# Optimization experiments

Hardware: AMD Instinct MI355X
Metric: run time of the kernel (lower is better)

The kernel has to match this reference:

```python
import jax, jax.numpy as jnp
import numpy as np

P = 524288          # total sampled points
N_RAYS = 4096       # rays
N_FREQ = 5
N_FREQ_VIEW = 3
ACT_SHIFT = float(np.log(1.0 / (1.0 - 0.1) - 1.0))  # alpha_init = 0.1
INTERVAL = 0.5      # stepsize * voxel_size_ratio


def sin_emb(x, n_freq):
    # x: (M,3) -> (M, 3 + 6*n_freq): [x, sin(2^i x), cos(2^i x)]
    freqs = 2.0 ** jnp.arange(n_freq, dtype=x.dtype)
    parts = [x]
    for f in freqs:
        parts.append(jnp.sin(f * x))
        parts.append(jnp.cos(f * x))
    return jnp.concatenate(parts, axis=1)


def _pipeline(sampling_coor, sampling_view, raw_density, ray_id,
              wb0, bb0, wb1, bb1, wb2, bb2,
              wa0, ba0, wa1, ba1, wa2, ba2,
              w_lat, b_lat, w_view, b_view, w_c0, b_c0, w_c1, b_c1):
    relu = jax.nn.relu
    emb = sin_emb(sampling_coor, N_FREQ)                    # (P, 33)
    view_emb = sin_emb(sampling_view, N_FREQ_VIEW)[ray_id]  # (P, 21)
    # Decoder_woslot (K == 1)
    h = relu(emb @ wb0 + bb0)
    h = relu(h @ wb1 + bb1)
    h = relu(h @ wb2 + bb2)
    h = jnp.concatenate([emb, h], axis=1)                   # skip: (P, 97)
    h = relu(h @ wa0 + ba0)
    h = relu(h @ wa1 + ba1)
    h = relu(h @ wa2 + ba2)
    latent = h @ w_lat + b_lat                              # (P, 64)
    hv = relu(jnp.concatenate([latent, view_emb], axis=1) @ w_view + b_view)
    rgb_raw = relu(hv @ w_c0 + b_c0) @ w_c1 + b_c1          # (P, 3)
    rgb = (jnp.tanh(rgb_raw) + 1.0) * 0.5
    sigma = jax.nn.softplus(raw_density[0] + ACT_SHIFT)     # (P,)
    # Raw2Alpha: alpha = 1 - exp(-sigma*interval); hence log(1-alpha) = -sigma*interval
    alpha = 1.0 - jnp.exp(-sigma * INTERVAL)
    log_t = -sigma * INTERVAL
    # Alphas2Weights: per-ray exclusive cumprod of (1-alpha); ray_id is sorted
    cl = jnp.cumsum(log_t)
    excl = cl - log_t                                        # exclusive global cumsum
    base = jax.ops.segment_max(excl, ray_id, num_segments=N_RAYS)  # value at each ray start
    T = jnp.exp(excl - base[ray_id])                         # transmittance
    weights = T * alpha                                      # (P,)
    alphainv_last = jnp.exp(jax.ops.segment_sum(log_t, ray_id, num_segments=N_RAYS))
    # composite with white background
    rgb_marched = (jax.ops.segment_sum(weights[:, None] * rgb, ray_id, num_segments=N_RAYS)
                   + alphainv_last[:, None])
    return rgb_marched                                       # (N_RAYS, 3)


def setup_inputs() -> dict:
    key = jax.random.key(0)
    ks = iter(jax.random.split(key, 40))

    def w(fi, fo):
        return jax.random.normal(next(ks), (fi, fo), jnp.float32) / np.sqrt(fi).astype(np.float32)

    inp = {
        'sampling_coor': jax.random.normal(next(ks), (P, 3), jnp.float32),
        'sampling_view': jax.random.normal(next(ks), (N_RAYS, 3), jnp.float32),
        'raw_density': jax.random.normal(next(ks), (1, P), jnp.float32),
        'ray_id': jnp.sort(jax.random.randint(next(ks), (P,), 0, N_RAYS, jnp.int32)),
        'wb0': w(33, 64), 'bb0': jnp.zeros((64,), jnp.float32),
        'wb1': w(64, 64), 'bb1': jnp.zeros((64,), jnp.float32),
        'wb2': w(64, 64), 'bb2': jnp.zeros((64,), jnp.float32),
        'wa0': w(97, 64), 'ba0': jnp.zeros((64,), jnp.float32),
        'wa1': w(64, 64), 'ba1': jnp.zeros((64,), jnp.float32),
        'wa2': w(64, 64), 'ba2': jnp.zeros((64,), jnp.float32),
        'w_lat': w(64, 64), 'b_lat': jnp.zeros((64,), jnp.float32),
        'w_view': w(85, 32), 'b_view': jnp.zeros((32,), jnp.float32),
        'w_c0': w(32, 16), 'b_c0': jnp.zeros((16,), jnp.float32),
        'w_c1': w(16, 3), 'b_c1': jnp.zeros((3,), jnp.float32),
    }
    return inp


def reference(sampling_coor, sampling_view, raw_density, ray_id,
              wb0, bb0, wb1, bb1, wb2, bb2,
              wa0, ba0, wa1, ba1, wa2, ba2,
              w_lat, b_lat, w_view, b_view, w_c0, b_c0, w_c1, b_c1):
    return _pipeline(sampling_coor, sampling_view, raw_density, ray_id,
                     wb0, bb0, wb1, bb1, wb2, bb2,
                     wa0, ba0, wa1, ba1, wa2, ba2,
                     w_lat, b_lat, w_view, b_view, w_c0, b_c0, w_c1, b_c1)
```

## Files before the change

### kernel.cpp

```cpp
#include <hip/hip_runtime.h>
#include <math.h>

#define NPTS  524288
#define NRAYS 4096
#define ACT_SHIFT_F (-2.1972245773362196f)
#define INTERVAL_F  0.5f

typedef _Float16 f16x8  __attribute__((ext_vector_type(8)));
typedef __fp16   fp16x2 __attribute__((ext_vector_type(2)));
typedef float    f32x4  __attribute__((ext_vector_type(4)));
typedef float    f32x16 __attribute__((ext_vector_type(16)));
typedef int      i32x2  __attribute__((ext_vector_type(2)));
typedef unsigned u32;
typedef unsigned u32x4  __attribute__((ext_vector_type(4)));

#define MFMA32(a,b,c) __builtin_amdgcn_mfma_f32_32x32x16_f16((a),(b),(c),0,0,0)

#define FB0_H   0
#define FD1_H   3072
#define FD2_H   7168
#define FA0_H   11264
#define FD3_H   18432
#define FD4_H   22528
#define FLAT_H  26624
#define LDSW_H  30720
#define FVIEW_H 30720
#define FC0_H   33792
#define BTAB_H  34816
#define VTAB_H  35840
#define RAYTAB_H 166912

#define PREP_W    34816
#define PREP_BT   (PREP_W + 512)
#define PREP_IDS  (PREP_BT + NRAYS)
#define PREP_TOTAL (PREP_IDS + NPTS)

#define UB0  0
#define UD1  1536
#define UD2  3584
#define UA0  5632
#define UD3  9216
#define UD4  11264
#define ULAT 13312
#define LDS_U32 15360

__device__ __forceinline__ u32 pk(float a, float b) {
    fp16x2 h = __builtin_amdgcn_cvt_pkrtz(a, b);
    return __builtin_bit_cast(u32, h);
}

__device__ __forceinline__ void plswap(u32 &x, u32 &y) {
    i32x2 r = __builtin_amdgcn_permlane32_swap((int)x, (int)y, false, false);
    x = (u32)r[0]; y = (u32)r[1];
}

template<bool RELU>
__device__ __forceinline__ f16x8 reluq(f16x8 v) {
    if (RELU) {
        f16x8 z = {};
        return __builtin_elementwise_max(v, z);
    }
    return v;
}

template<bool RELU>
__device__ __forceinline__ void d2b(f32x16 a, f16x8 &blo, f16x8 &bhi) {
    u32 p0 = pk(a[0],a[1]),   p1 = pk(a[2],a[3]);
    u32 p2 = pk(a[4],a[5]),   p3 = pk(a[6],a[7]);
    plswap(p0, p2); plswap(p1, p3);
    u32x4 lo = {p0, p1, p2, p3};
    blo = reluq<RELU>(__builtin_bit_cast(f16x8, lo));
    u32 p4 = pk(a[8],a[9]),   p5 = pk(a[10],a[11]);
    u32 p6 = pk(a[12],a[13]), p7 = pk(a[14],a[15]);
    plswap(p4, p6); plswap(p5, p7);
    u32x4 hw = {p4, p5, p6, p7};
    bhi = reluq<RELU>(__builtin_bit_cast(f16x8, hw));
}

__device__ __forceinline__ f16x8 ldf(const u32* __restrict__ swl, int imm) {
    return __builtin_bit_cast(f16x8, *(const u32x4*)(swl + imm));
}

extern "C" __global__ void __launch_bounds__(256)
prep_weights(const float* __restrict__ wb0, const float* __restrict__ bb0,
             const float* __restrict__ wb1, const float* __restrict__ bb1,
             const float* __restrict__ wb2, const float* __restrict__ bb2,
             const float* __restrict__ wa0, const float* __restrict__ ba0,
             const float* __restrict__ wa1, const float* __restrict__ ba1,
             const float* __restrict__ wa2, const float* __restrict__ ba2,
             const float* __restrict__ wlat, const float* __restrict__ blat,
             const float* __restrict__ wview, const float* __restrict__ bview,
             const float* __restrict__ wc0, const float* __restrict__ bc0,
             const float* __restrict__ view, const int* __restrict__ ray_id,
             _Float16* __restrict__ pool)
{
    const int id = blockIdx.x * 256 + threadIdx.x;
    if (id >= PREP_TOTAL) return;

    if (id < PREP_W) {
        int r = id; float v = 0.f;
        if (r < 33792) {
            const float* W; int base, MT;
            if      (r < 3072)  { W = wb0;  base = 0;     MT = 2; }
            else if (r < 7168)  { W = wb1;  base = 3072;  MT = 2; }
            else if (r < 11264) { W = wb2;  base = 7168;  MT = 2; }
            else if (r < 18432) { W = wa0;  base = 11264; MT = 2; }
            else if (r < 22528) { W = wa1;  base = 18432; MT = 2; }
            else if (r < 26624) { W = wa2;  base = 22528; MT = 2; }
            else if (r < 30720) { W = wlat; base = 26624; MT = 2; }
            else                { W = wview;base = 30720; MT = 1; }
            const int e    = r - base;
            const int j    = e & 7;
            const int lane = (e >> 3) & 63;
            const int col  = lane & 31, hi = lane >> 5;
            int kc, mt;
            if (MT == 2) { kc = e >> 10; mt = (e >> 9) & 1; }
            else         { kc = e >> 9;  mt = 0; }
            const int of = mt * 32 + col;
            const int k  = kc * 16 + hi * 8 + j;
            if (W == wb0) {
                if (k < 3) v = wb0[k*64+of];
                else if (k >= 4 && k < 34) v = wb0[(k-1)*64+of];
            } else if (W == wa0) {
                if (k < 3) v = wa0[k*64+of];
                else if (k >= 4 && k < 34) v = wa0[(k-1)*64+of];
                else if (k >= 48 && k < 112) v = wa0[(k-15)*64+of];
            } else if (W == wview) {
                if (k < 64) v = wview[k*32+of];
                else { int s = k - 64;
                       if (s < 3) v = wview[(64+s)*32+of];
                       else if (s >= 4 && s < 22) v = wview[(63+s)*32+of]; }
            } else {
                if (k < 64) v = W[k*64+of];
            }
            pool[id] = (_Float16)v;
        } else {
            const int e = r - 33792;
            const int j = e & 7;
            const int lane = (e >> 3) & 63;
            const int col = lane & 31, hi = lane >> 5;
            const int kc = e >> 9;
            const int k = kc * 16 + hi * 8 + j;
            float v2 = (col < 16 && k < 32) ? wc0[k*16+col] : 0.f;
            pool[id] = (_Float16)v2;
        }
        return;
    }

    if (id < PREP_BT) {
        float* bt = (float*)(pool + BTAB_H);
        const int e = id - PREP_W; float v = 0.f;
        if (e < 448) {
            int l = e >> 6, rem = e & 63;
            int mt = rem >> 5, hi2 = (rem >> 4) & 1, q = rem & 15;
            int row = (q & 3) + 8*(q >> 2) + 4*hi2 + 32*mt;
            const float* src[7] = { bb0, bb1, bb2, ba0, ba1, ba2, blat };
            v = src[l][row];
        } else if (e < 480) {
            int t = e - 448, hi2 = t >> 4, q = t & 15;
            int row = (q & 3) + 8*(q >> 2) + 4*hi2;
            v = bview[row];
        } else if (e < 496) {
            int t = e - 480, hi2 = t >> 3, q = t & 7;
            int row = (q & 3) + 8*(q >> 2) + 4*hi2;
            v = bc0[row];
        }
        bt[e] = v;
        return;
    }

    if (id < PREP_IDS) {
        const int ray = id - PREP_BT;
        const float vx = view[3*ray+0], vy = view[3*ray+1], vz = view[3*ray+2];
        u32 w_[16];
        w_[0] = pk(vx, vy); w_[1] = pk(vz, 0.f);
#pragma unroll
        for (int f = 0; f < 3; ++f) {
            const float fac = (float)(1 << f);
            float sx = __sinf(fac*vx), cx = __cosf(fac*vx);
            float sy = __sinf(fac*vy), cy = __cosf(fac*vy);
            float sz = __sinf(fac*vz), cz = __cosf(fac*vz);
            w_[2+3*f+0] = pk(sx,sy); w_[2+3*f+1] = pk(sz,cx); w_[2+3*f+2] = pk(cy,cz);
        }
#pragma unroll
        for (int i = 11; i < 16; ++i) w_[i] = 0u;
        u32* dst = (u32*)(pool + VTAB_H) + ray * 16;
#pragma unroll
        for (int i = 0; i < 4; ++i)
            ((u32x4*)dst)[i] = (u32x4){w_[4*i], w_[4*i+1], w_[4*i+2], w_[4*i+3]};
        return;
    }

    {
        const int p = id - PREP_IDS;
        int* tab = (int*)(pool + RAYTAB_H);
        const int cur  = ray_id[p];
        const int prev = (p == 0) ? -1 : ray_id[p-1];
        for (int r = prev + 1; r <= cur; ++r) tab[r] = p;
        if (p == NPTS - 1)
            for (int r = cur + 1; r <= NRAYS; ++r) tab[r] = NPTS;
    }
}

__device__ __forceinline__ void loadBV(f32x16 (&bv)[2], const float* __restrict__ bt,
                                       int l, int hi) {
#pragma unroll
    for (int mt = 0; mt < 2; ++mt) {
        const float* p = bt + l*64 + (mt*2 + hi)*16;
#pragma unroll
        for (int i = 0; i < 4; ++i) {
            f32x4 v = *(const f32x4*)(p + 4*i);
#pragma unroll
            for (int s = 0; s < 4; ++s) bv[mt][4*i + s] = v[s];
        }
    }
}

template<bool RELU>
__device__ __forceinline__ void denseL(const u32* __restrict__ swl, int base,
                                       const f32x16 (&bv)[2], f16x8 (&b)[4][4]) {
    f16x8 W[2][4];
#pragma unroll
    for (int mt = 0; mt < 2; ++mt)
#pragma unroll
        for (int kc = 0; kc < 4; ++kc)
            W[mt][kc] = ldf(swl, base + (kc*2 + mt)*256);
#pragma unroll
    for (int t = 0; t < 4; ++t) {
        f32x16 a0 = MFMA32(W[0][0], b[t][0], bv[0]);
        f32x16 a1 = MFMA32(W[1][0], b[t][0], bv[1]);
#pragma unroll
        for (int kc = 1; kc < 4; ++kc) {
            a0 = MFMA32(W[0][kc], b[t][kc], a0);
            a1 = MFMA32(W[1][kc], b[t][kc], a1);
        }
        d2b<RELU>(a0, b[t][0], b[t][1]);
        d2b<RELU>(a1, b[t][2], b[t][3]);
    }
}

extern "C" __global__ void __launch_bounds__(512, 2)
mlp_mfma(const float* __restrict__ coor, const int* __restrict__ ray_id,
         const float* __restrict__ wc1, const float* __restrict__ bc1,
         const _Float16* __restrict__ pool, _Float16* __restrict__ rgb)
{
    __shared__ __align__(16) u32 sw[LDS_U32];
    const int tid  = threadIdx.x;
    const int lane = tid & 63;
    const int wv   = tid >> 6;
    const int col  = lane & 31;
    const int hi   = lane >> 5;
    const int wbase = blockIdx.x * 1024 + wv * 128;

    {
        const u32x4* pw = (const u32x4*)pool;
        u32x4* dw = (u32x4*)sw;
#pragma unroll
        for (int i = tid; i < LDS_U32/4; i += 512) dw[i] = pw[i];
    }

    int rid[4];
#pragma unroll
    for (int t = 0; t < 4; ++t) rid[t] = ray_id[wbase + 32*t + col];

    f16x8 E[4][3];
#pragma unroll
    for (int s = 0; s < 2; ++s) {
        const int pt = wbase + s*64 + lane;
        const float x = coor[3*pt+0], y = coor[3*pt+1], z = coor[3*pt+2];
        u32 w_[17];
        w_[0] = pk(x, y); w_[1] = pk(z, 0.f);
#pragma unroll
        for (int f = 0; f < 5; ++f) {
            const float fac = (float)(1 << f);
            float sx = __sinf(fac*x), cx = __cosf(fac*x);
            float sy = __sinf(fac*y), cy = __cosf(fac*y);
            float sz = __sinf(fac*z), cz = __cosf(fac*z);
            w_[2+3*f+0] = pk(sx,sy); w_[2+3*f+1] = pk(sz,cx); w_[2+3*f+2] = pk(cy,cz);
        }
#pragma unroll
        for (int kc = 0; kc < 2; ++kc) {
            u32 xw[4], yw[4];
#pragma unroll
            for (int i = 0; i < 4; ++i) {
                xw[i] = w_[kc*8 + i]; yw[i] = w_[kc*8 + 4 + i];
                plswap(xw[i], yw[i]);
            }
            u32x4 lo = {xw[0], xw[1], xw[2], xw[3]};
            u32x4 hw = {yw[0], yw[1], yw[2], yw[3]};
            E[2*s  ][kc] = __builtin_bit_cast(f16x8, lo);
            E[2*s+1][kc] = __builtin_bit_cast(f16x8, hw);
        }
        u32 X = w_[16], Y = 0u;
        plswap(X, Y);
        u32x4 e2a = {X, 0u, 0u, 0u}, e2b = {Y, 0u, 0u, 0u};
        E[2*s  ][2] = __builtin_bit_cast(f16x8, e2a);
        E[2*s+1][2] = __builtin_bit_cast(f16x8, e2b);
    }
    __syncthreads();

    const u32* swl = sw + lane * 4;
    const float* bt = (const float*)(pool + BTAB_H);

    f16x8 b[4][4];
    f32x16 bv[2];

    {
        f16x8 W[2][3];
#pragma unroll
        for (int mt = 0; mt < 2; ++mt)
#pragma unroll
            for (int kc = 0; kc < 3; ++kc)
                W[mt][kc] = ldf(swl, UB0 + (kc*2 + mt)*256);
        loadBV(bv, bt, 0, hi);
#pragma unroll
        for (int t = 0; t < 4; ++t) {
            f32x16 a0 = MFMA32(W[0][0], E[t][0], bv[0]);
            f32x16 a1 = MFMA32(W[1][0], E[t][0], bv[1]);
            a0 = MFMA32(W[0][1], E[t][1], a0);
            a1 = MFMA32(W[1][1], E[t][1], a1);
            a0 = MFMA32(W[0][2], E[t][2], a0);
            a1 = MFMA32(W[1][2], E[t][2], a1);
            d2b<true>(a0, b[t][0], b[t][1]);
            d2b<true>(a1, b[t][2], b[t][3]);
        }
    }

    loadBV(bv, bt, 1, hi);
    denseL<true>(swl, UD1, bv, b);
    loadBV(bv, bt, 2, hi);
    denseL<true>(swl, UD2, bv, b);

    {
        f16x8 We[2][3], Wh[2][4];
#pragma unroll
        for (int mt = 0; mt < 2; ++mt) {
#pragma unroll
            for (int kc = 0; kc < 3; ++kc)
                We[mt][kc] = ldf(swl, UA0 + (kc*2 + mt)*256);
#pragma unroll
            for (int kc = 0; kc < 4; ++kc)
                Wh[mt][kc] = ldf(swl, UA0 + ((kc+3)*2 + mt)*256);
        }
        loadBV(bv, bt, 3, hi);
#pragma unroll
        for (int t = 0; t < 4; ++t) {
            f32x16 a0 = MFMA32(We[0][0], E[t][0], bv[0]);
            f32x16 a1 = MFMA32(We[1][0], E[t][0], bv[1]);
            a0 = MFMA32(We[0][1], E[t][1], a0);
            a1 = MFMA32(We[1][1], E[t][1], a1);
            a0 = MFMA32(We[0][2], E[t][2], a0);
            a1 = MFMA32(We[1][2], E[t][2], a1);
#pragma unroll
            for (int kc = 0; kc < 4; ++kc) {
                a0 = MFMA32(Wh[0][kc], b[t][kc], a0);
                a1 = MFMA32(Wh[1][kc], b[t][kc], a1);
            }
            d2b<true>(a0, b[t][0], b[t][1]);
            d2b<true>(a1, b[t][2], b[t][3]);
        }
    }

    loadBV(bv, bt, 4, hi);
    denseL<true>(swl, UD3, bv, b);
    loadBV(bv, bt, 5, hi);
    denseL<true>(swl, UD4, bv, b);

    const _Float16* vtab = pool + VTAB_H;
    f16x8 VE[4][2];
#pragma unroll
    for (int t = 0; t < 4; ++t)
#pragma unroll
        for (int kc = 0; kc < 2; ++kc)
            VE[t][kc] = *(const f16x8*)(vtab + rid[t]*32 + kc*16 + hi*8);

    loadBV(bv, bt, 6, hi);
    denseL<false>(swl, ULAT, bv, b);

    {
        f16x8 Wv[6];
#pragma unroll
        for (int kc = 0; kc < 6; ++kc)
            Wv[kc] = *(const f16x8*)(pool + FVIEW_H + (kc*64 + lane)*8);
        f32x16 bvv;
        {
            const float* p = bt + 448 + hi*16;
#pragma unroll
            for (int i = 0; i < 4; ++i) {
                f32x4 v = *(const f32x4*)(p + 4*i);
#pragma unroll
                for (int s = 0; s < 4; ++s) bvv[4*i + s] = v[s];
            }
        }
#pragma unroll
        for (int t = 0; t < 4; ++t) {
            f32x16 a = MFMA32(Wv[0], b[t][0], bvv);
#pragma unroll
            for (int kc = 1; kc < 4; ++kc) a = MFMA32(Wv[kc], b[t][kc], a);
            a = MFMA32(Wv[4], VE[t][0], a);
            a = MFMA32(Wv[5], VE[t][1], a);
            d2b<true>(a, b[t][0], b[t][1]);
        }
    }

    {
        f16x8 Wc[2];
#pragma unroll
        for (int kc = 0; kc < 2; ++kc)
            Wc[kc] = *(const f16x8*)(pool + FC0_H + (kc*64 + lane)*8);

        f32x16 C;
        {
            f32x4 c0a = *(const f32x4*)(bt + 480 + hi*8);
            f32x4 c0b = *(const f32x4*)(bt + 480 + hi*8 + 4);
#pragma unroll
            for (int s = 0; s < 4; ++s) {
                C[s] = c0a[s]; C[4+s] = c0b[s]; C[8+s] = 0.f; C[12+s] = 0.f;
            }
        }

        float wl[24];
        {
            f32x4 w0 = *(const f32x4*)(wc1 + 12*hi);
            f32x4 w1 = *(const f32x4*)(wc1 + 12*hi + 4);
            f32x4 w2 = *(const f32x4*)(wc1 + 12*hi + 8);
            f32x4 w3 = *(const f32x4*)(wc1 + 24 + 12*hi);
            f32x4 w4 = *(const f32x4*)(wc1 + 24 + 12*hi + 4);
            f32x4 w5 = *(const f32x4*)(wc1 + 24 + 12*hi + 8);
#pragma unroll
            for (int s = 0; s < 4; ++s) {
                wl[s]    = w0[s]; wl[4+s]  = w1[s]; wl[8+s]  = w2[s];
                wl[12+s] = w3[s]; wl[16+s] = w4[s]; wl[20+s] = w5[s];
            }
        }
        const float bo0 = bc1[0], bo1 = bc1[1], bo2 = bc1[2];

#pragma unroll
        for (int t = 0; t < 4; ++t) {
            f32x16 a = MFMA32(Wc[0], b[t][0], C);
            a = MFMA32(Wc[1], b[t][1], a);
            float hc[8];
#pragma unroll
            for (int i = 0; i < 8; ++i) hc[i] = fmaxf(a[i], 0.f);

            float r0 = 0.f, r1 = 0.f, r2 = 0.f;
#pragma unroll
            for (int q = 0; q < 4; ++q) {
                r0 = fmaf(hc[q], wl[3*q+0], fmaf(hc[4+q], wl[12+3*q+0], r0));
                r1 = fmaf(hc[q], wl[3*q+1], fmaf(hc[4+q], wl[12+3*q+1], r1));
                r2 = fmaf(hc[q], wl[3*q+2], fmaf(hc[4+q], wl[12+3*q+2], r2));
            }
            r0 += __shfl_xor(r0, 32);
            r1 += __shfl_xor(r1, 32);
            r2 += __shfl_xor(r2, 32);
            if (hi == 0) {
                const float K2 = 2.8853900817779268f;
                float e0 = exp2f(K2 * (r0 + bo0));
                float e1 = exp2f(K2 * (r1 + bo1));
                float e2 = exp2f(K2 * (r2 + bo2));
                float v0 = 1.f - __builtin_amdgcn_rcpf(e0 + 1.f);
                float v1 = 1.f - __builtin_amdgcn_rcpf(e1 + 1.f);
                float v2 = 1.f - __builtin_amdgcn_rcpf(e2 + 1.f);
                const int pt = wbase + 32*t + col;
                rgb[3*pt+0] = (_Float16)v0;
                rgb[3*pt+1] = (_Float16)v1;
                rgb[3*pt+2] = (_Float16)v2;
            }
        }
    }
}

extern "C" __global__ void __launch_bounds__(256)
composite(const float* __restrict__ raw_density,
          const int*   __restrict__ rtab,
          const _Float16* __restrict__ rgb,
          float*       __restrict__ out)
{
    const int lane = threadIdx.x & 63;
    const int ray  = blockIdx.x * 4 + (threadIdx.x >> 6);

    const int start = rtab[ray];
    const int end   = rtab[ray + 1];

    float carry = 0.0f, a0 = 0.0f, a1 = 0.0f, a2 = 0.0f;

    for (int base = start; base < end; base += 64) {
        const int  idx   = base + lane;
        const bool valid = idx < end;

        float lt = 0.0f, alpha = 0.0f;
        if (valid) {
            const float xx  = raw_density[idx] + ACT_SHIFT_F;
            const float sig = fmaxf(xx, 0.0f) + log1pf(expf(-fabsf(xx)));
            lt    = -sig * INTERVAL_F;
            alpha = 1.0f - expf(lt);
        }

        float incl = lt;
#pragma unroll
        for (int d = 1; d < 64; d <<= 1) {
            const float n = __shfl_up(incl, d);
            if (lane >= d) incl += n;
        }

        const float T = expf(carry + (incl - lt));
        if (valid) {
            const float w = T * alpha;
            a0 = fmaf(w, (float)rgb[3*idx+0], a0);
            a1 = fmaf(w, (float)rgb[3*idx+1], a1);
            a2 = fmaf(w, (float)rgb[3*idx+2], a2);
        }
        carry += __shfl(incl, 63);
    }

#pragma unroll
    for (int d = 32; d > 0; d >>= 1) {
        a0 += __shfl_xor(a0, d);
        a1 += __shfl_xor(a1, d);
        a2 += __shfl_xor(a2, d);
    }

    if (lane == 0) {
        const float ainv = expf(carry);
        out[3*ray+0] = a0 + ainv;
        out[3*ray+1] = a1 + ainv;
        out[3*ray+2] = a2 + ainv;
    }
}

extern "C" void kernel_launch(void* const* d_in, const int* in_sizes, int n_in,
                              void* d_out, int out_size, void* d_ws, size_t ws_size,
                              hipStream_t stream) {
    const float* coor        = (const float*)d_in[0];
    const float* view        = (const float*)d_in[1];
    const float* raw_density = (const float*)d_in[2];
    const int*   ray_id      = (const int*)  d_in[3];
    const float* wb0  = (const float*)d_in[4];  const float* bb0  = (const float*)d_in[5];
    const float* wb1  = (const float*)d_in[6];  const float* bb1  = (const float*)d_in[7];
    const float* wb2  = (const float*)d_in[8];  const float* bb2  = (const float*)d_in[9];
    const float* wa0  = (const float*)d_in[10]; const float* ba0  = (const float*)d_in[11];
    const float* wa1  = (const float*)d_in[12]; const float* ba1  = (const float*)d_in[13];
    const float* wa2  = (const float*)d_in[14]; const float* ba2  = (const float*)d_in[15];
    const float* wlat = (const float*)d_in[16]; const float* blat = (const float*)d_in[17];
    const float* wvw  = (const float*)d_in[18]; const float* bvw  = (const float*)d_in[19];
    const float* wc0  = (const float*)d_in[20]; const float* bc0  = (const float*)d_in[21];
    const float* wc1  = (const float*)d_in[22]; const float* bc1  = (const float*)d_in[23];

    _Float16* rgb  = (_Float16*)d_ws;
    _Float16* pool = (_Float16*)((char*)d_ws + (size_t)NPTS * 3 * 2);
    const int* rtab = (const int*)(pool + RAYTAB_H);

    prep_weights<<<(PREP_TOTAL + 255) / 256, 256, 0, stream>>>(
        wb0, bb0, wb1, bb1, wb2, bb2, wa0, ba0, wa1, ba1, wa2, ba2,
        wlat, blat, wvw, bvw, wc0, bc0, view, ray_id, pool);

    mlp_mfma<<<NPTS / 1024, 512, 0, stream>>>(
        coor, ray_id, wc1, bc1, pool, rgb);

    composite<<<NRAYS / 4, 256, 0, stream>>>(raw_density, rtab, rgb, (float*)d_out);
}
```

Measured before the change: 52.01 us.

## Stage bias table in LDS, raise MFMA priority, stagger waves with sleep

The bias table is copied into shared memory next to the weights, so per-layer bias loads come from LDS instead of global memory. MFMA loops are wrapped in s_setprio(1)/s_setprio(0) so math-heavy waves get issue priority. Waves are staggered with different s_sleep delays after the barrier so their MFMA and load phases interleave. The changes add 2 KB of LDS per block and some idle time at the start of each wave.

```diff
diff --git a/kernel.cpp b/kernel.cpp
--- a/kernel.cpp
+++ b/kernel.cpp
@@ -16,14 +16,6 @@
 
 #define MFMA32(a,b,c) __builtin_amdgcn_mfma_f32_32x32x16_f16((a),(b),(c),0,0,0)
 
-#define FB0_H   0
-#define FD1_H   3072
-#define FD2_H   7168
-#define FA0_H   11264
-#define FD3_H   18432
-#define FD4_H   22528
-#define FLAT_H  26624
-#define LDSW_H  30720
 #define FVIEW_H 30720
 #define FC0_H   33792
 #define BTAB_H  34816
@@ -42,7 +34,9 @@
 #define UD3  9216
 #define UD4  11264
 #define ULAT 13312
-#define LDS_U32 15360
+#define WLDS_U32 15360
+#define BT_U32   512
+#define LDS_U32 (WLDS_U32 + BT_U32)
 
 __device__ __forceinline__ u32 pk(float a, float b) {
     fp16x2 h = __builtin_amdgcn_cvt_pkrtz(a, b);
@@ -202,11 +196,11 @@
     }
 }
 
-__device__ __forceinline__ void loadBV(f32x16 (&bv)[2], const float* __restrict__ bt,
+__device__ __forceinline__ void loadBV(f32x16 (&bv)[2], const float* __restrict__ btl,
                                        int l, int hi) {
 #pragma unroll
     for (int mt = 0; mt < 2; ++mt) {
-        const float* p = bt + l*64 + (mt*2 + hi)*16;
+        const float* p = btl + l*64 + (mt*2 + hi)*16;
 #pragma unroll
         for (int i = 0; i < 4; ++i) {
             f32x4 v = *(const f32x4*)(p + 4*i);
@@ -225,6 +219,7 @@
 #pragma unroll
         for (int kc = 0; kc < 4; ++kc)
             W[mt][kc] = ldf(swl, base + (kc*2 + mt)*256);
+    __builtin_amdgcn_s_setprio(1);
 #pragma unroll
     for (int t = 0; t < 4; ++t) {
         f32x16 a0 = MFMA32(W[0][0], b[t][0], bv[0]);
@@ -237,6 +232,7 @@
         d2b<RELU>(a0, b[t][0], b[t][1]);
         d2b<RELU>(a1, b[t][2], b[t][3]);
     }
+    __builtin_amdgcn_s_setprio(0);
 }
 
 extern "C" __global__ void __launch_bounds__(512, 2)
@@ -256,7 +252,8 @@
         const u32x4* pw = (const u32x4*)pool;
         u32x4* dw = (u32x4*)sw;
 #pragma unroll
-        for (int i = tid; i < LDS_U32/4; i += 512) dw[i] = pw[i];
+        for (int i = tid; i < WLDS_U32/4; i += 512) dw[i] = pw[i];
+        if (tid < 128) dw[WLDS_U32/4 + tid] = pw[17408/4 + tid];
     }
 
     int rid[4];
@@ -299,8 +296,15 @@
     }
     __syncthreads();
 
+    {
+        const int w3 = wv & 3;
+        if (w3 == 1)      __builtin_amdgcn_s_sleep(8);
+        else if (w3 == 2) __builtin_amdgcn_s_sleep(16);
+        else if (w3 == 3) __builtin_amdgcn_s_sleep(24);
+    }
+
     const u32* swl = sw + lane * 4;
-    const float* bt = (const float*)(pool + BTAB_H);
+    const float* btl = (const float*)(sw + WLDS_U32);
 
     f16x8 b[4][4];
     f32x16 bv[2];
@@ -312,7 +316,8 @@
 #pragma unroll
             for (int kc = 0; kc < 3; ++kc)
                 W[mt][kc] = ldf(swl, UB0 + (kc*2 + mt)*256);
-        loadBV(bv, bt, 0, hi);
+        loadBV(bv, btl, 0, hi);
+        __builtin_amdgcn_s_setprio(1);
 #pragma unroll
         for (int t = 0; t < 4; ++t) {
             f32x16 a0 = MFMA32(W[0][0], E[t][0], bv[0]);
@@ -324,11 +329,12 @@
             d2b<true>(a0, b[t][0], b[t][1]);
             d2b<true>(a1, b[t][2], b[t][3]);
         }
-    }
-
-    loadBV(bv, bt, 1, hi);
+        __builtin_amdgcn_s_setprio(0);
+    }
+
+    loadBV(bv, btl, 1, hi);
     denseL<true>(swl, UD1, bv, b);
-    loadBV(bv, bt, 2, hi);
+    loadBV(bv, btl, 2, hi);
     denseL<true>(swl, UD2, bv, b);
 
     {
@@ -342,7 +348,8 @@
             for (int kc = 0; kc < 4; ++kc)
                 Wh[mt][kc] = ldf(swl, UA0 + ((kc+3)*2 + mt)*256);
         }
-        loadBV(bv, bt, 3, hi);
+        loadBV(bv, btl, 3, hi);
+        __builtin_amdgcn_s_setprio(1);
 #pragma unroll
         for (int t = 0; t < 4; ++t) {
             f32x16 a0 = MFMA32(We[0][0], E[t][0], bv[0]);
@@ -359,11 +366,12 @@
             d2b<true>(a0, b[t][0], b[t][1]);
             d2b<true>(a1, b[t][2], b[t][3]);
         }
-    }
-
-    loadBV(bv, bt, 4, hi);
+        __builtin_amdgcn_s_setprio(0);
+    }
+
+    loadBV(bv, btl, 4, hi);
     denseL<true>(swl, UD3, bv, b);
-    loadBV(bv, bt, 5, hi);
+    loadBV(bv, btl, 5, hi);
     denseL<true>(swl, UD4, bv, b);
 
     const _Float16* vtab = pool + VTAB_H;
@@ -374,7 +382,7 @@
         for (int kc = 0; kc < 2; ++kc)
             VE[t][kc] = *(const f16x8*)(vtab + rid[t]*32 + kc*16 + hi*8);
 
-    loadBV(bv, bt, 6, hi);
+    loadBV(bv, btl, 6, hi);
     denseL<false>(swl, ULAT, bv, b);
 
     {
@@ -384,7 +392,7 @@
             Wv[kc] = *(const f16x8*)(pool + FVIEW_H + (kc*64 + lane)*8);
         f32x16 bvv;
         {
-            const float* p = bt + 448 + hi*16;
+            const float* p = btl + 448 + hi*16;
 #pragma unroll
             for (int i = 0; i < 4; ++i) {
                 f32x4 v = *(const f32x4*)(p + 4*i);
@@ -392,6 +400,7 @@
                 for (int s = 0; s < 4; ++s) bvv[4*i + s] = v[s];
             }
         }
+        __builtin_amdgcn_s_setprio(1);
 #pragma unroll
         for (int t = 0; t < 4; ++t) {
             f32x16 a = MFMA32(Wv[0], b[t][0], bvv);
@@ -401,6 +410,7 @@
             a = MFMA32(Wv[5], VE[t][1], a);
             d2b<true>(a, b[t][0], b[t][1]);
         }
+        __builtin_amdgcn_s_setprio(0);
     }
 
     {
@@ -411,8 +421,8 @@
 
         f32x16 C;
         {
-            f32x4 c0a = *(const f32x4*)(bt + 480 + hi*8);
-            f32x4 c0b = *(const f32x4*)(bt + 480 + hi*8 + 4);
+            f32x4 c0a = *(const f32x4*)(btl + 480 + hi*8);
+            f32x4 c0b = *(const f32x4*)(btl + 480 + hi*8 + 4);
 #pragma unroll
             for (int s = 0; s < 4; ++s) {
                 C[s] = c0a[s]; C[4+s] = c0b[s]; C[8+s] = 0.f; C[12+s] = 0.f;
```

Measured after the change: 54.01 us. +3.8%, slower.
